# Kernel tuning notes

Measured on AMD Instinct MI355X. Metric: run time of the kernel, lower is better.

The kernel has to match this reference:

```python
import jax, jax.numpy as jnp
import numpy as np

N_NODES = 100000
N_EDGES = 1600000
D_IN = 128
D_HID = 128
D_OUT = 40


def _linear_init(key, fan_in, fan_out):
    # torch nn.Linear default: U(-1/sqrt(fan_in), 1/sqrt(fan_in)) for W and b
    kw, kb = jax.random.split(key)
    bound = 1.0 / np.sqrt(fan_in)
    W = jax.random.uniform(kw, (fan_in, fan_out), jnp.float32, -bound, bound)
    b = jax.random.uniform(kb, (fan_out,), jnp.float32, -bound, bound)
    return W, b


def setup_inputs() -> dict:
    key = jax.random.key(0)
    ks = jax.random.split(key, 8)
    x = jax.random.normal(ks[0], (N_NODES, D_IN), jnp.float32)
    edges = jax.random.randint(ks[1], (2, N_EDGES), 0, N_NODES, jnp.int64)
    # layer 0: MLP(128 -> 128 -> 128)
    W1_0, b1_0 = _linear_init(ks[2], D_IN, D_HID)
    W2_0, b2_0 = _linear_init(ks[3], D_HID, D_HID)
    # layer 1: MLP(128 -> 128 -> 128)
    W1_1, b1_1 = _linear_init(ks[4], D_HID, D_HID)
    W2_1, b2_1 = _linear_init(ks[5], D_HID, D_HID)
    # layer 2: MLP(128 -> 128 -> 40)
    W1_2, b1_2 = _linear_init(ks[6], D_HID, D_HID)
    W2_2, b2_2 = _linear_init(ks[7], D_HID, D_OUT)
    eps = jnp.zeros(())  # GINConv train_eps=True initializes eps=0
    return {
        "x": x, "edges": edges,
        "W1_0": W1_0, "b1_0": b1_0, "W2_0": W2_0, "b2_0": b2_0, "eps_0": eps,
        "W1_1": W1_1, "b1_1": b1_1, "W2_1": W2_1, "b2_1": b2_1, "eps_1": eps,
        "W1_2": W1_2, "b1_2": b1_2, "W2_2": W2_2, "b2_2": b2_2, "eps_2": eps,
    }


def _gin_conv(x, src, dst, eps, W1, b1, W2, b2):
    # sum-aggregate neighbor features: out_i = MLP((1+eps)*x_i + sum_{j->i} x_j)
    aggr = jax.ops.segment_sum(x[src], dst, num_segments=x.shape[0])
    h = (1.0 + eps) * x + aggr
    h = jnp.maximum(h @ W1 + b1, 0.0)  # MLP layer 1 + ReLU
    return h @ W2 + b2                  # MLP layer 2


def reference(x, edges,
              W1_0, b1_0, W2_0, b2_0, eps_0,
              W1_1, b1_1, W2_1, b2_1, eps_1,
              W1_2, b1_2, W2_2, b2_2, eps_2):
    src, dst = edges[0], edges[1]
    # dropout is identity at inference (training=False)
    h = jax.nn.relu(_gin_conv(x, src, dst, eps_0, W1_0, b1_0, W2_0, b2_0))
    h = jax.nn.relu(_gin_conv(h, src, dst, eps_1, W1_1, b1_1, W2_1, b2_1))
    o = _gin_conv(h, src, dst, eps_2, W1_2, b1_2, W2_2, b2_2)
    return jax.nn.log_softmax(o, axis=1)
```

## Files before the change

### kernel.cpp

```cpp
#include <hip/hip_runtime.h>
#include <stdint.h>

typedef __attribute__((ext_vector_type(8))) short short8;
typedef __attribute__((ext_vector_type(4))) float float4v;

__device__ __forceinline__ float bf2f(unsigned short s) {
    union { unsigned int u; float f; } c; c.u = ((unsigned int)s) << 16; return c.f;
}
__device__ __forceinline__ unsigned short f2bf(float f) {
    union { float f; unsigned int u; } c; c.f = f;
    unsigned int x = c.u;
    unsigned int r = x + 0x7fffu + ((x >> 16) & 1u);
    return (unsigned short)(r >> 16);
}
__device__ __forceinline__ void unpack2(unsigned int u, float& lo, float& hi) {
    union { unsigned int uu; float ff; } a, b;
    a.uu = u << 16;
    b.uu = u & 0xffff0000u;
    lo = a.ff; hi = b.ff;
}

__global__ __launch_bounds__(256) void bs_count(const int* __restrict__ dst, int nE,
                                                int* __restrict__ bucketCnt) {
    __shared__ int c[512];
    int t = threadIdx.x;
    for (int i = t; i < 512; i += 256) c[i] = 0;
    __syncthreads();
    int base = blockIdx.x * 4096;
    for (int i = t; i < 4096; i += 256) {
        int e = base + i;
        if (e < nE) atomicAdd(&c[dst[e] >> 8], 1);
    }
    __syncthreads();
    for (int i = t; i < 512; i += 256)
        if (c[i]) atomicAdd(&bucketCnt[i], c[i]);
}

__global__ __launch_bounds__(512) void bs_scan(const int* __restrict__ bucketCnt,
                                               int* __restrict__ bucketBase,
                                               int* __restrict__ bucketCur,
                                               int* __restrict__ off, int M, int nE) {
    __shared__ int s[512];
    int t = threadIdx.x;
    int v = bucketCnt[t];
    s[t] = v;
    __syncthreads();
    for (int o = 1; o < 512; o <<= 1) {
        int x = (t >= o) ? s[t - o] : 0;
        __syncthreads();
        s[t] += x;
        __syncthreads();
    }
    bucketBase[t] = s[t] - v;
    bucketCur[t] = s[t] - v;
    if (t == 511) bucketBase[512] = s[511];
    if (t == 0) off[M] = nE;
}

__global__ __launch_bounds__(512) void bs_scatter(const int* __restrict__ src,
                                                  const int* __restrict__ dst, int nE,
                                                  int* __restrict__ bucketCur,
                                                  unsigned int* __restrict__ ebuf) {
    __shared__ int cnt[512];
    __shared__ int excl[512];
    __shared__ int chunk[512];
    __shared__ unsigned int buf[4096];
    __shared__ unsigned short bkt[4096];
    int t = threadIdx.x;
    cnt[t] = 0;
    __syncthreads();
    int base = blockIdx.x * 4096;
    int n = nE - base; if (n > 4096) n = 4096;
    unsigned int pk[8]; int bk[8]; int rk[8];
#pragma unroll
    for (int u = 0; u < 8; ++u) {
        int i = t + u * 512;
        if (i < n) {
            int e = base + i;
            int d = dst[e];
            int b = d >> 8;
            bk[u] = b;
            pk[u] = (unsigned int)src[e] | ((unsigned int)(d & 255) << 17);
            rk[u] = atomicAdd(&cnt[b], 1);
        } else bk[u] = -1;
    }
    __syncthreads();
    excl[t] = cnt[t];
    __syncthreads();
    for (int o = 1; o < 512; o <<= 1) {
        int x = (t >= o) ? excl[t - o] : 0;
        __syncthreads();
        excl[t] += x;
        __syncthreads();
    }
    int ex = excl[t] - cnt[t];
    __syncthreads();
    excl[t] = ex;
    if (cnt[t]) chunk[t] = atomicAdd(&bucketCur[t], cnt[t]);
    __syncthreads();
#pragma unroll
    for (int u = 0; u < 8; ++u) {
        if (bk[u] >= 0) {
            int lp = excl[bk[u]] + rk[u];
            buf[lp] = pk[u];
            bkt[lp] = (unsigned short)bk[u];
        }
    }
    __syncthreads();
    for (int i = t; i < n; i += 512) {
        int b = bkt[i];
        ebuf[chunk[b] + (i - excl[b])] = buf[i];
    }
}

__global__ __launch_bounds__(512) void bs_build(const unsigned int* __restrict__ ebuf,
                                                const int* __restrict__ bucketBase,
                                                int* __restrict__ off,
                                                int* __restrict__ esrc, int M) {
    __shared__ int cnt[256];
    __shared__ int excl[256];
    __shared__ int obuf[5120];
    int t = threadIdx.x, b = blockIdx.x;
    int base = bucketBase[b];
    int n = bucketBase[b + 1] - base;
    if (t < 256) cnt[t] = 0;
    __syncthreads();
    unsigned int pk[10]; int dl[10]; int rk[10];
#pragma unroll
    for (int u = 0; u < 10; ++u) {
        int i = t + u * 512;
        if (i < n) {
            unsigned int p = ebuf[base + i];
            pk[u] = p;
            int d = (p >> 17) & 255;
            dl[u] = d;
            rk[u] = atomicAdd(&cnt[d], 1);
        } else dl[u] = -1;
    }
    __syncthreads();
    if (t < 256) excl[t] = cnt[t];
    __syncthreads();
    for (int o = 1; o < 256; o <<= 1) {
        int x = (t < 256 && t >= o) ? excl[t - o] : 0;
        __syncthreads();
        if (t < 256) excl[t] += x;
        __syncthreads();
    }
    if (t < 256) {
        int ex = excl[t] - cnt[t];
        int node = b * 256 + t;
        if (node < M) off[node] = base + ex;
        excl[t] = ex;
    }
    __syncthreads();
#pragma unroll
    for (int u = 0; u < 10; ++u) {
        if (dl[u] >= 0) {
            int lp = excl[dl[u]] + rk[u];
            if (lp < 5120) obuf[lp] = (int)(pk[u] & 0x1FFFF);
        }
    }
    __syncthreads();
    for (int i = t; i < n; i += 512) esrc[base + i] = obuf[i];
}

struct Prep {
    const float* W[6];
    unsigned short* hi[6];
    const float4* xin;
    uint2* xout;
    int n4;
};

__global__ __launch_bounds__(256) void k_prep(Prep p) {
    int b = blockIdx.x;
    if (b < 344) {
        int mat = b >> 6;
        int rel = b - mat * 64;
        int NPAD = (mat == 5) ? 48 : 128;
        int N = (mat == 5) ? 40 : 128;
        int idx = rel * 256 + threadIdx.x;
        if (idx >= NPAD * 128) return;
        int n = idx >> 7, k = idx & 127;
        float w = (n < N) ? p.W[mat][k * N + n] : 0.f;
        p.hi[mat][idx] = f2bf(w);
    } else {
        int i = (b - 344) * 256 + threadIdx.x;
        if (i >= p.n4) return;
        float4 v = p.xin[i];
        uint2 o;
        o.x = ((unsigned int)f2bf(v.y) << 16) | f2bf(v.x);
        o.y = ((unsigned int)f2bf(v.w) << 16) | f2bf(v.z);
        p.xout[i] = o;
    }
}

__device__ __forceinline__ void acc8(uint4 v, float* s) {
    float a, b;
    unpack2(v.x, a, b); s[0] += a; s[1] += b;
    unpack2(v.y, a, b); s[2] += a; s[3] += b;
    unpack2(v.z, a, b); s[4] += a; s[5] += b;
    unpack2(v.w, a, b); s[6] += a; s[7] += b;
}

__global__ __launch_bounds__(256) void k_aggr(const uint4* __restrict__ Hin,
                                              const int* __restrict__ off,
                                              const int* __restrict__ esrc,
                                              const float* __restrict__ epsp,
                                              uint4* __restrict__ Ahi, int M) {
    int w = threadIdx.x >> 6, lane = threadIdx.x & 63;
    int li = lane & 15, q = lane >> 4;
    int node = blockIdx.x * 16 + w * 4 + q;
    if (node >= M) return;
    float ep = 1.0f + epsp[0];
    uint4 ow = Hin[node * 16 + li];
    float s[8] = {0.f, 0.f, 0.f, 0.f, 0.f, 0.f, 0.f, 0.f};
    int i = off[node], e = off[node + 1];
    for (; i + 8 <= e; i += 8) {
        uint4 v[8];
#pragma unroll
        for (int j = 0; j < 8; ++j) v[j] = Hin[esrc[i + j] * 16 + li];
#pragma unroll
        for (int j = 0; j < 8; ++j) acc8(v[j], s);
    }
    if (i < e) {
        int last = e - 1;
        uint4 v[8];
#pragma unroll
        for (int j = 0; j < 8; ++j) {
            int idx = i + j;
            int cl = idx < last ? idx : last;
            v[j] = Hin[esrc[cl] * 16 + li];
        }
#pragma unroll
        for (int j = 0; j < 8; ++j) {
            bool ok = (i + j) < e;
            uint4 u;
            u.x = ok ? v[j].x : 0u;
            u.y = ok ? v[j].y : 0u;
            u.z = ok ? v[j].z : 0u;
            u.w = ok ? v[j].w : 0u;
            acc8(u, s);
        }
    }
    float o[8];
    unpack2(ow.x, o[0], o[1]);
    unpack2(ow.y, o[2], o[3]);
    unpack2(ow.z, o[4], o[5]);
    unpack2(ow.w, o[6], o[7]);
#pragma unroll
    for (int k = 0; k < 8; ++k) s[k] = ep * o[k] + s[k];
    uint4 r;
    r.x = ((unsigned int)f2bf(s[1]) << 16) | f2bf(s[0]);
    r.y = ((unsigned int)f2bf(s[3]) << 16) | f2bf(s[2]);
    r.z = ((unsigned int)f2bf(s[5]) << 16) | f2bf(s[4]);
    r.w = ((unsigned int)f2bf(s[7]) << 16) | f2bf(s[6]);
    Ahi[node * 16 + li] = r;
}

template <int NT2, bool LOGITS>
__global__ __launch_bounds__(256, 3) void k_mlp(const unsigned short* __restrict__ AhiS,
                                                const unsigned short* __restrict__ W1h,
                                                const float* __restrict__ B1,
                                                const unsigned short* __restrict__ W2h,
                                                const float* __restrict__ B2,
                                                unsigned short* __restrict__ HOut,
                                                float* __restrict__ LOut, int M) {
    __shared__ short wbuf[128 * 136];
    __shared__ short slab[4][16 * 136];
    int t = threadIdx.x, w = t >> 6, lane = t & 63;
    int lm = lane & 15, lg = lane >> 4;
    int rbase = blockIdx.x * 128;

    for (int i = t * 8; i < 128 * 128; i += 2048) {
        int n = i >> 7, k = i & 127;
        *(short8*)&wbuf[n * 136 + k] = *(const short8*)(W1h + i);
    }
    __syncthreads();

    short8 hh[2][4];
#pragma unroll
    for (int t2 = 0; t2 < 2; ++t2) {
        int r0 = rbase + t2 * 64 + w * 16;
        if (r0 < M) {
            const short* Ah = (const short*)AhiS + (r0 + lm) * 128 + lg * 8;
            short8 ah[4];
#pragma unroll
            for (int kb = 0; kb < 4; ++kb) ah[kb] = *(const short8*)(Ah + kb * 32);
            float4v acc[8];
#pragma unroll
            for (int nt = 0; nt < 8; ++nt) acc[nt] = (float4v){0.f, 0.f, 0.f, 0.f};
#pragma unroll
            for (int nt = 0; nt < 8; ++nt) {
#pragma unroll
                for (int kb = 0; kb < 4; ++kb) {
                    short8 wh = *(const short8*)&wbuf[(nt * 16 + lm) * 136 + kb * 32 + lg * 8];
                    acc[nt] = __builtin_amdgcn_mfma_f32_16x16x32_bf16(ah[kb], wh, acc[nt], 0, 0, 0);
                }
            }
#pragma unroll
            for (int nt = 0; nt < 8; ++nt) {
                float b = B1[nt * 16 + lm];
#pragma unroll
                for (int r = 0; r < 4; ++r) {
                    float v = acc[nt][r] + b;
                    v = v > 0.f ? v : 0.f;
                    slab[w][(lg * 4 + r) * 136 + nt * 16 + lm] = (short)f2bf(v);
                }
            }
#pragma unroll
            for (int kb = 0; kb < 4; ++kb)
                hh[t2][kb] = *(const short8*)&slab[w][lm * 136 + kb * 32 + lg * 8];
        }
    }

    __syncthreads();
    for (int i = t * 8; i < NT2 * 16 * 128; i += 2048) {
        int n = i >> 7, k = i & 127;
        *(short8*)&wbuf[n * 136 + k] = *(const short8*)(W2h + i);
    }
    __syncthreads();

#pragma unroll
    for (int t2 = 0; t2 < 2; ++t2) {
        int r0 = rbase + t2 * 64 + w * 16;
        if (r0 >= M) continue;
        float4v acc2[NT2];
#pragma unroll
        for (int nt = 0; nt < NT2; ++nt) acc2[nt] = (float4v){0.f, 0.f, 0.f, 0.f};
#pragma unroll
        for (int nt = 0; nt < NT2; ++nt) {
#pragma unroll
            for (int kb = 0; kb < 4; ++kb) {
                short8 wh = *(const short8*)&wbuf[(nt * 16 + lm) * 136 + kb * 32 + lg * 8];
                acc2[nt] = __builtin_amdgcn_mfma_f32_16x16x32_bf16(hh[t2][kb], wh, acc2[nt], 0, 0, 0);
            }
        }
        if (!LOGITS) {
#pragma unroll
            for (int nt = 0; nt < NT2; ++nt) {
                int col = nt * 16 + lm;
                float b = B2[col];
#pragma unroll
                for (int r = 0; r < 4; ++r) {
                    float v = acc2[nt][r] + b;
                    v = v > 0.f ? v : 0.f;
                    HOut[(r0 + lg * 4 + r) * 128 + col] = f2bf(v);
                }
            }
        } else {
            float vv[NT2][4];
#pragma unroll
            for (int nt = 0; nt < NT2; ++nt) {
                int col = nt * 16 + lm;
                bool valid = col < 40;
                float b = valid ? B2[col] : 0.f;
#pragma unroll
                for (int r = 0; r < 4; ++r)
                    vv[nt][r] = valid ? (acc2[nt][r] + b) : -1e30f;
            }
#pragma unroll
            for (int r = 0; r < 4; ++r) {
                float m = vv[0][r];
#pragma unroll
                for (int nt = 1; nt < NT2; ++nt) m = fmaxf(m, vv[nt][r]);
#pragma unroll
                for (int o = 8; o >= 1; o >>= 1) m = fmaxf(m, __shfl_xor(m, o, 64));
                float s = 0.f;
#pragma unroll
                for (int nt = 0; nt < NT2; ++nt)
                    s += (vv[nt][r] > -1e29f) ? expf(vv[nt][r] - m) : 0.f;
#pragma unroll
                for (int o = 8; o >= 1; o >>= 1) s += __shfl_xor(s, o, 64);
                float ls = m + logf(s);
                int row = r0 + lg * 4 + r;
#pragma unroll
                for (int nt = 0; nt < NT2; ++nt) {
                    int col = nt * 16 + lm;
                    if (col < 40) LOut[row * 40 + col] = vv[nt][r] - ls;
                }
            }
        }
    }
}

extern "C" void kernel_launch(void* const* d_in, const int* in_sizes, int n_in,
                              void* d_out, int out_size, void* d_ws, size_t ws_size,
                              hipStream_t stream) {
    const float* x    = (const float*)d_in[0];
    const int*   edges = (const int*)d_in[1];
    const float* eps0 = (const float*)d_in[6];
    const float* eps1 = (const float*)d_in[11];
    const float* eps2 = (const float*)d_in[16];
    const float* B1[3] = {(const float*)d_in[3], (const float*)d_in[8], (const float*)d_in[13]};
    const float* B2[3] = {(const float*)d_in[5], (const float*)d_in[10], (const float*)d_in[15]};

    int M  = in_sizes[0] / 128;
    int nE = in_sizes[1] / 2;
    const int* e_src = edges;
    const int* e_dst = edges + nE;

    char* ws = (char*)d_ws;
    size_t o = 0;
    auto alloc = [&](size_t bytes) {
        size_t p = o;
        o = (o + bytes + 511) & ~(size_t)511;
        return ws + p;
    };
    int* bucketCnt  = (int*)alloc(512 * 4);
    int* bucketBase = (int*)alloc(513 * 4);
    int* bucketCur  = (int*)alloc(512 * 4);
    int* off  = (int*)alloc((size_t)(M + 1) * 4);
    int* esrc = (int*)alloc((size_t)nE * 4);
    unsigned int* ebuf = (unsigned int*)alloc((size_t)nE * 4);

    Prep pp;
    pp.W[0] = (const float*)d_in[2];  pp.W[1] = (const float*)d_in[4];
    pp.W[2] = (const float*)d_in[7];  pp.W[3] = (const float*)d_in[9];
    pp.W[4] = (const float*)d_in[12]; pp.W[5] = (const float*)d_in[14];
    for (int m = 0; m < 6; ++m) {
        int npad = (m == 5) ? 48 : 128;
        pp.hi[m] = (unsigned short*)alloc((size_t)npad * 128 * 2);
    }
    unsigned short* xb  = (unsigned short*)alloc((size_t)M * 128 * 2);
    unsigned short* Ahi = (unsigned short*)alloc((size_t)M * 128 * 2);
    unsigned short* Hb  = (unsigned short*)alloc((size_t)M * 128 * 2);
    pp.xin = (const float4*)x;
    pp.xout = (uint2*)xb;
    pp.n4 = M * 32;
    (void)ws_size; (void)n_in; (void)out_size;

    hipMemsetAsync(bucketCnt, 0, 512 * 4, stream);
    int nChunk = (nE + 4095) / 4096;
    int nBk = (M + 255) / 256;
    bs_count<<<nChunk, 256, 0, stream>>>(e_dst, nE, bucketCnt);
    bs_scan<<<1, 512, 0, stream>>>(bucketCnt, bucketBase, bucketCur, off, M, nE);
    bs_scatter<<<nChunk, 512, 0, stream>>>(e_src, e_dst, nE, bucketCur, ebuf);
    bs_build<<<nBk, 512, 0, stream>>>(ebuf, bucketBase, off, esrc, M);
    k_prep<<<344 + (pp.n4 + 255) / 256, 256, 0, stream>>>(pp);

    int gA = (M + 15) / 16;
    int gG = (M + 127) / 128;

    k_aggr<<<gA, 256, 0, stream>>>((const uint4*)xb, off, esrc, eps0, (uint4*)Ahi, M);
    k_mlp<8, false><<<gG, 256, 0, stream>>>(Ahi, pp.hi[0], B1[0],
                                            pp.hi[1], B2[0], Hb, nullptr, M);
    k_aggr<<<gA, 256, 0, stream>>>((const uint4*)Hb, off, esrc, eps1, (uint4*)Ahi, M);
    k_mlp<8, false><<<gG, 256, 0, stream>>>(Ahi, pp.hi[2], B1[1],
                                            pp.hi[3], B2[1], Hb, nullptr, M);
    k_aggr<<<gA, 256, 0, stream>>>((const uint4*)Hb, off, esrc, eps2, (uint4*)Ahi, M);
    k_mlp<3, true><<<gG, 256, 0, stream>>>(Ahi, pp.hi[4], B1[2],
                                           pp.hi[5], B2[2], nullptr,
                                           (float*)d_out, M);
}
```

Baseline: 408.4 us.

## Compute transposed MLP tiles so hidden activations stay in registers without LDS slab

Swaps the MFMA operand order so the first GEMM produces a transposed tile whose accumulator layout matches the B-operand layout of a 16x16x16 bf16 MFMA. The hidden activations then feed the second GEMM straight from registers, which removes the per-wave LDS slab round trip and lets occupancy rise to 4 blocks. Epilogues now use vectorized bias loads and packed row-contiguous stores, and the log-softmax reduction needs only two shuffles per row. The second GEMM uses the smaller-K MFMA with more instructions, and the raised launch bound may add register pressure.

Result: no change. 404.2 us (-1.0%).

```diff
diff --git a/kernel.cpp b/kernel.cpp
--- a/kernel.cpp
+++ b/kernel.cpp
@@ -2,6 +2,7 @@
 #include <stdint.h>
 
 typedef __attribute__((ext_vector_type(8))) short short8;
+typedef __attribute__((ext_vector_type(4))) short short4v;
 typedef __attribute__((ext_vector_type(4))) float float4v;
 
 __device__ __forceinline__ float bf2f(unsigned short s) {
@@ -259,7 +260,7 @@
 }
 
 template <int NT2, bool LOGITS>
-__global__ __launch_bounds__(256, 3) void k_mlp(const unsigned short* __restrict__ AhiS,
+__global__ __launch_bounds__(256, 4) void k_mlp(const unsigned short* __restrict__ AhiS,
                                                 const unsigned short* __restrict__ W1h,
                                                 const float* __restrict__ B1,
                                                 const unsigned short* __restrict__ W2h,
@@ -267,7 +268,6 @@
                                                 unsigned short* __restrict__ HOut,
                                                 float* __restrict__ LOut, int M) {
     __shared__ short wbuf[128 * 136];
-    __shared__ short slab[4][16 * 136];
     int t = threadIdx.x, w = t >> 6, lane = t & 63;
     int lm = lane & 15, lg = lane >> 4;
     int rbase = blockIdx.x * 128;
@@ -278,39 +278,41 @@
     }
     __syncthreads();
 
-    short8 hh[2][4];
+    short4v h2[2][8];
+    bool act[2];
 #pragma unroll
     for (int t2 = 0; t2 < 2; ++t2) {
         int r0 = rbase + t2 * 64 + w * 16;
-        if (r0 < M) {
-            const short* Ah = (const short*)AhiS + (r0 + lm) * 128 + lg * 8;
-            short8 ah[4];
-#pragma unroll
-            for (int kb = 0; kb < 4; ++kb) ah[kb] = *(const short8*)(Ah + kb * 32);
-            float4v acc[8];
-#pragma unroll
-            for (int nt = 0; nt < 8; ++nt) acc[nt] = (float4v){0.f, 0.f, 0.f, 0.f};
+        act[t2] = (r0 < M);
+        if (act[t2]) {
+            const short* Xp = (const short*)AhiS + (r0 + lm) * 128 + lg * 8;
+            short8 xf[4];
+#pragma unroll
+            for (int kb = 0; kb < 4; ++kb) xf[kb] = *(const short8*)(Xp + kb * 32);
+            float4v acc1[8];
+#pragma unroll
+            for (int nt = 0; nt < 8; ++nt) acc1[nt] = (float4v){0.f, 0.f, 0.f, 0.f};
 #pragma unroll
             for (int nt = 0; nt < 8; ++nt) {
 #pragma unroll
                 for (int kb = 0; kb < 4; ++kb) {
-                    short8 wh = *(const short8*)&wbuf[(nt * 16 + lm) * 136 + kb * 32 + lg * 8];
-                    acc[nt] = __builtin_amdgcn_mfma_f32_16x16x32_bf16(ah[kb], wh, acc[nt], 0, 0, 0);
+                    short8 wf = *(const short8*)&wbuf[(nt * 16 + lm) * 136 + kb * 32 + lg * 8];
+                    acc1[nt] = __builtin_amdgcn_mfma_f32_16x16x32_bf16(wf, xf[kb], acc1[nt], 0, 0, 0);
                 }
             }
 #pragma unroll
             for (int nt = 0; nt < 8; ++nt) {
-                float b = B1[nt * 16 + lm];
-#pragma unroll
-                for (int r = 0; r < 4; ++r) {
-                    float v = acc[nt][r] + b;
-                    v = v > 0.f ? v : 0.f;
-                    slab[w][(lg * 4 + r) * 136 + nt * 16 + lm] = (short)f2bf(v);
-                }
+                float4 b1 = *(const float4*)(B1 + nt * 16 + lg * 4);
+                float v0 = acc1[nt][0] + b1.x; v0 = v0 > 0.f ? v0 : 0.f;
+                float v1 = acc1[nt][1] + b1.y; v1 = v1 > 0.f ? v1 : 0.f;
+                float v2 = acc1[nt][2] + b1.z; v2 = v2 > 0.f ? v2 : 0.f;
+                float v3 = acc1[nt][3] + b1.w; v3 = v3 > 0.f ? v3 : 0.f;
+                h2[t2][nt] = (short4v){(short)f2bf(v0), (short)f2bf(v1),
+                                       (short)f2bf(v2), (short)f2bf(v3)};
             }
-#pragma unroll
-            for (int kb = 0; kb < 4; ++kb)
-                hh[t2][kb] = *(const short8*)&slab[w][lm * 136 + kb * 32 + lg * 8];
+        } else {
+#pragma unroll
+            for (int nt = 0; nt < 8; ++nt) h2[t2][nt] = (short4v){0, 0, 0, 0};
         }
     }
 
@@ -321,63 +323,75 @@
     }
     __syncthreads();
 
+    float4v acc2[2][NT2];
+#pragma unroll
+    for (int t2 = 0; t2 < 2; ++t2)
+#pragma unroll
+        for (int ot = 0; ot < NT2; ++ot) acc2[t2][ot] = (float4v){0.f, 0.f, 0.f, 0.f};
+#pragma unroll
+    for (int ot = 0; ot < NT2; ++ot) {
+#pragma unroll
+        for (int nt = 0; nt < 8; ++nt) {
+            short4v wf = *(const short4v*)&wbuf[(ot * 16 + lm) * 136 + nt * 16 + lg * 4];
+#pragma unroll
+            for (int t2 = 0; t2 < 2; ++t2)
+                acc2[t2][ot] = __builtin_amdgcn_mfma_f32_16x16x16bf16_1k(wf, h2[t2][nt],
+                                                                         acc2[t2][ot], 0, 0, 0);
+        }
+    }
+
 #pragma unroll
     for (int t2 = 0; t2 < 2; ++t2) {
-        int r0 = rbase + t2 * 64 + w * 16;
-        if (r0 >= M) continue;
-        float4v acc2[NT2];
-#pragma unroll
-        for (int nt = 0; nt < NT2; ++nt) acc2[nt] = (float4v){0.f, 0.f, 0.f, 0.f};
-#pragma unroll
-        for (int nt = 0; nt < NT2; ++nt) {
-#pragma unroll
-            for (int kb = 0; kb < 4; ++kb) {
-                short8 wh = *(const short8*)&wbuf[(nt * 16 + lm) * 136 + kb * 32 + lg * 8];
-                acc2[nt] = __builtin_amdgcn_mfma_f32_16x16x32_bf16(hh[t2][kb], wh, acc2[nt], 0, 0, 0);
-            }
-        }
+        if (!act[t2]) continue;
+        int row = rbase + t2 * 64 + w * 16 + lm;
         if (!LOGITS) {
 #pragma unroll
-            for (int nt = 0; nt < NT2; ++nt) {
-                int col = nt * 16 + lm;
-                float b = B2[col];
-#pragma unroll
-                for (int r = 0; r < 4; ++r) {
-                    float v = acc2[nt][r] + b;
-                    v = v > 0.f ? v : 0.f;
-                    HOut[(r0 + lg * 4 + r) * 128 + col] = f2bf(v);
-                }
+            for (int ot = 0; ot < NT2; ++ot) {
+                float4 b2 = *(const float4*)(B2 + ot * 16 + lg * 4);
+                float v0 = acc2[t2][ot][0] + b2.x; v0 = v0 > 0.f ? v0 : 0.f;
+                float v1 = acc2[t2][ot][1] + b2.y; v1 = v1 > 0.f ? v1 : 0.f;
+                float v2 = acc2[t2][ot][2] + b2.z; v2 = v2 > 0.f ? v2 : 0.f;
+                float v3 = acc2[t2][ot][3] + b2.w; v3 = v3 > 0.f ? v3 : 0.f;
+                uint2 pk;
+                pk.x = ((unsigned int)f2bf(v1) << 16) | f2bf(v0);
+                pk.y = ((unsigned int)f2bf(v3) << 16) | f2bf(v2);
+                *(uint2*)(HOut + row * 128 + ot * 16 + lg * 4) = pk;
             }
         } else {
             float vv[NT2][4];
 #pragma unroll
-            for (int nt = 0; nt < NT2; ++nt) {
-                int col = nt * 16 + lm;
-                bool valid = col < 40;
-                float b = valid ? B2[col] : 0.f;
+            for (int ot = 0; ot < NT2; ++ot) {
+                int ub = ot * 16 + lg * 4;
+                bool valid = ub <= 36;
+                float4 b2 = valid ? *(const float4*)(B2 + ub) : (float4){0.f, 0.f, 0.f, 0.f};
+                vv[ot][0] = valid ? acc2[t2][ot][0] + b2.x : -1e30f;
+                vv[ot][1] = valid ? acc2[t2][ot][1] + b2.y : -1e30f;
+                vv[ot][2] = valid ? acc2[t2][ot][2] + b2.z : -1e30f;
+                vv[ot][3] = valid ? acc2[t2][ot][3] + b2.w : -1e30f;
+            }
+            float m = -1e30f;
+#pragma unroll
+            for (int ot = 0; ot < NT2; ++ot)
+#pragma unroll
+                for (int r = 0; r < 4; ++r) m = fmaxf(m, vv[ot][r]);
+            m = fmaxf(m, __shfl_xor(m, 16, 64));
+            m = fmaxf(m, __shfl_xor(m, 32, 64));
+            float s = 0.f;
+#pragma unroll
+            for (int ot = 0; ot < NT2; ++ot)
 #pragma unroll
                 for (int r = 0; r < 4; ++r)
-                    vv[nt][r] = valid ? (acc2[nt][r] + b) : -1e30f;
-            }
-#pragma unroll
-            for (int r = 0; r < 4; ++r) {
-                float m = vv[0][r];
-#pragma unroll
-                for (int nt = 1; nt < NT2; ++nt) m = fmaxf(m, vv[nt][r]);
-#pragma unroll
-                for (int o = 8; o >= 1; o >>= 1) m = fmaxf(m, __shfl_xor(m, o, 64));
-                float s = 0.f;
-#pragma unroll
-                for (int nt = 0; nt < NT2; ++nt)
-                    s += (vv[nt][r] > -1e29f) ? expf(vv[nt][r] - m) : 0.f;
-#pragma unroll
-                for (int o = 8; o >= 1; o >>= 1) s += __shfl_xor(s, o, 64);
-                float ls = m + logf(s);
-                int row = r0 + lg * 4 + r;
-#pragma unroll
-                for (int nt = 0; nt < NT2; ++nt) {
-                    int col = nt * 16 + lm;
-                    if (col < 40) LOut[row * 40 + col] = vv[nt][r] - ls;
+                    s += (vv[ot][r] > -1e29f) ? expf(vv[ot][r] - m) : 0.f;
+            s += __shfl_xor(s, 16, 64);
+            s += __shfl_xor(s, 32, 64);
+            float ls = m + logf(s);
+#pragma unroll
+            for (int ot = 0; ot < NT2; ++ot) {
+                int ub = ot * 16 + lg * 4;
+                if (ub <= 36) {
+                    float4 outv = {vv[ot][0] - ls, vv[ot][1] - ls,
+                                   vv[ot][2] - ls, vv[ot][3] - ls};
+                    *(float4*)(LOut + row * 40 + ub) = outv;
                 }
             }
         }
```
